# Kernel tuning notes

Measured on AMD Instinct MI355X. Metric: run time of the kernel, lower is better.

The kernel has to match this reference:

```python
import jax, jax.numpy as jnp
import numpy as np

NUM_CODEBOOKS = 8
CODEBOOK_SIZE = 2048
CODEBOOK_DIM = 16
HIDDEN_SIZE = 2048
CODEC_VOCAB_START = 0
PAD_IDX = 0


def setup_inputs() -> dict:
    key = jax.random.key(0)
    k_ids, k_emb, k_w1, k_b1, k_w2, k_b2 = jax.random.split(key, 6)
    B, S = 4, 4096
    codec_input_ids = jax.random.randint(
        k_ids, (B, S), 0, NUM_CODEBOOKS * CODEBOOK_SIZE, dtype=jnp.int64
    )
    # frozen embedding table; padding_idx row is zero
    embed_table = jax.random.normal(
        k_emb, (NUM_CODEBOOKS * CODEBOOK_SIZE, CODEBOOK_DIM), dtype=jnp.float32
    )
    embed_table = embed_table.at[PAD_IDX].set(0.0)
    # per-codebook projector params (stacked over codebook axis k)
    s1 = 1.0 / np.sqrt(CODEBOOK_DIM)
    s2 = 1.0 / np.sqrt(HIDDEN_SIZE)
    W1 = jax.random.uniform(k_w1, (NUM_CODEBOOKS, CODEBOOK_DIM, HIDDEN_SIZE), jnp.float32, -s1, s1)
    b1 = jax.random.uniform(k_b1, (NUM_CODEBOOKS, HIDDEN_SIZE), jnp.float32, -s1, s1)
    W2 = jax.random.uniform(k_w2, (NUM_CODEBOOKS, HIDDEN_SIZE, HIDDEN_SIZE), jnp.float32, -s2, s2)
    b2 = jax.random.uniform(k_b2, (NUM_CODEBOOKS, HIDDEN_SIZE), jnp.float32, -s2, s2)
    return {
        "codec_input_ids": codec_input_ids,
        "embed_table": embed_table,
        "W1": W1,
        "b1": b1,
        "W2": W2,
        "b2": b2,
    }


def reference(codec_input_ids, embed_table, W1, b1, W2, b2):
    ids = codec_input_ids - CODEC_VOCAB_START          # [B, S]
    embeds = embed_table[ids]                          # [B, S, D]
    cb = ids // CODEBOOK_SIZE                          # which codebook each token belongs to
    out = jnp.zeros(ids.shape + (HIDDEN_SIZE,), dtype=embeds.dtype)
    # fixed small loop over structurally distinct per-codebook projectors;
    # disjoint masks cover all tokens, so masked accumulation == torch scatter
    for k in range(NUM_CODEBOOKS):
        h = jnp.einsum("bsd,dh->bsh", embeds, W1[k]) + b1[k]
        h = jax.nn.gelu(h, approximate=False)          # torch nn.GELU default = exact
        h = jnp.einsum("bsh,hg->bsg", h, W2[k]) + b2[k]
        out = out + jnp.where((cb == k)[..., None], h, 0.0)
    return out
```

## Files before the change

### kernel.cpp

```cpp
#include <hip/hip_runtime.h>
#include <hip/hip_bf16.h>
#include <stdint.h>

#define NUM_CB   8
#define CB_BITS  11
#define DIM      16
#define HS       2048
#define NTOK     16384

#define BM 256
#define BN 256
#define BK 64
#define NKT (HS / BK)
#define MAXT 72
#define GEMM_GRID (8 * MAXT)

#define OFF_CUR    0u
#define OFF_NT     64u
#define OFF_GS     128u
#define OFF_TCB    256u
#define OFF_TROW   1024u
#define OFF_TVAL   2048u
#define OFF_PERM   4096u
#define OFF_H      69632u
#define OFF_W2T    67178496u
#define WS_NEED    134287360u

typedef __attribute__((ext_vector_type(8))) short s16x8;
typedef __attribute__((ext_vector_type(4))) float f32x4;

__device__ __forceinline__ void load_lds16(const void* g, const void* l) {
    __builtin_amdgcn_global_load_lds(
        (const __attribute__((address_space(1))) uint32_t*)g,
        (__attribute__((address_space(3))) uint32_t*)(void*)(uintptr_t)l, 16, 0, 0);
}

extern "C" __global__ void k_countplan(const int* __restrict__ ids,
                                       uint32_t* __restrict__ cur, uint32_t* __restrict__ numT,
                                       uint32_t* __restrict__ tcb, uint32_t* __restrict__ trow,
                                       uint32_t* __restrict__ tval, uint32_t* __restrict__ gstart) {
    __shared__ uint32_t hist[NUM_CB];
    __shared__ uint32_t s_tcb[MAXT], s_trow[MAXT], s_tval[MAXT];
    __shared__ uint32_t s_gs[NUM_CB], s_nt;
    const int tid = threadIdx.x;
    if (tid < NUM_CB) { hist[tid] = 0; cur[tid] = 0; }
    __syncthreads();
    uint32_t c0=0,c1=0,c2=0,c3=0,c4=0,c5=0,c6=0,c7=0;
    const int4* v4 = (const int4*)ids;
    for (int i = tid; i < NTOK / 4; i += 1024) {
        int4 v = v4[i];
        uint32_t a = (uint32_t)v.x >> CB_BITS, b = (uint32_t)v.y >> CB_BITS;
        uint32_t cc = (uint32_t)v.z >> CB_BITS, d = (uint32_t)v.w >> CB_BITS;
        c0 += (a==0)+(b==0)+(cc==0)+(d==0);  c1 += (a==1)+(b==1)+(cc==1)+(d==1);
        c2 += (a==2)+(b==2)+(cc==2)+(d==2);  c3 += (a==3)+(b==3)+(cc==3)+(d==3);
        c4 += (a==4)+(b==4)+(cc==4)+(d==4);  c5 += (a==5)+(b==5)+(cc==5)+(d==5);
        c6 += (a==6)+(b==6)+(cc==6)+(d==6);  c7 += (a==7)+(b==7)+(cc==7)+(d==7);
    }
    #pragma unroll
    for (int off = 32; off > 0; off >>= 1) {
        c0 += __shfl_down(c0, off); c1 += __shfl_down(c1, off);
        c2 += __shfl_down(c2, off); c3 += __shfl_down(c3, off);
        c4 += __shfl_down(c4, off); c5 += __shfl_down(c5, off);
        c6 += __shfl_down(c6, off); c7 += __shfl_down(c7, off);
    }
    if ((tid & 63) == 0) {
        if (c0) atomicAdd(&hist[0], c0); if (c1) atomicAdd(&hist[1], c1);
        if (c2) atomicAdd(&hist[2], c2); if (c3) atomicAdd(&hist[3], c3);
        if (c4) atomicAdd(&hist[4], c4); if (c5) atomicAdd(&hist[5], c5);
        if (c6) atomicAdd(&hist[6], c6); if (c7) atomicAdd(&hist[7], c7);
    }
    __syncthreads();
    if (tid == 0) {
        uint32_t ps = 0, nt = 0;
        for (int k = 0; k < NUM_CB; ++k) {
            s_gs[k] = ps;
            uint32_t c = hist[k];
            uint32_t tiles = (c + BM - 1) / BM;
            for (uint32_t m = 0; m < tiles; ++m) {
                s_tcb[nt] = (uint32_t)k;
                s_trow[nt] = ps + m * BM;
                uint32_t rem = c - m * BM;
                s_tval[nt] = rem < BM ? rem : BM;
                ++nt;
            }
            ps += c;
        }
        s_nt = nt;
    }
    __syncthreads();
    const uint32_t nt = s_nt;
    if (tid < MAXT) {
        tcb[tid]  = (tid < (int)nt) ? s_tcb[tid] : 0u;
        trow[tid] = (tid < (int)nt) ? s_trow[tid] : 0u;
        tval[tid] = (tid < (int)nt) ? s_tval[tid] : 0u;
    }
    if (tid < NUM_CB) gstart[tid] = s_gs[tid];
    if (tid == 0) *numT = nt;
}

extern "C" __global__ void k_assign(const int* __restrict__ ids, const uint32_t* __restrict__ gstart,
                                    uint32_t* __restrict__ cur, uint32_t* __restrict__ perm) {
    __shared__ uint32_t lh[NUM_CB], lbase[NUM_CB];
    const int tid = threadIdx.x;
    const int t = blockIdx.x * 256 + tid;
    if (tid < NUM_CB) lh[tid] = 0;
    __syncthreads();
    const int cb = (uint32_t)ids[t] >> CB_BITS;
    atomicAdd(&lh[cb], 1u);
    __syncthreads();
    if (tid < NUM_CB) {
        lbase[tid] = lh[tid] ? atomicAdd(&cur[tid], lh[tid]) : 0u;
        lh[tid] = 0;
    }
    __syncthreads();
    const uint32_t r = atomicAdd(&lh[cb], 1u);
    perm[gstart[cb] + lbase[cb] + r] = (uint32_t)t;
}

extern "C" __global__ void k_hbuild(const int* __restrict__ ids, const float* __restrict__ emb,
                                    const float* __restrict__ W1, const float* __restrict__ b1,
                                    const uint32_t* __restrict__ numT, const uint32_t* __restrict__ tcb,
                                    const uint32_t* __restrict__ trow, const uint32_t* __restrict__ tval,
                                    const uint32_t* __restrict__ perm, __hip_bfloat16* __restrict__ H) {
    if (blockIdx.x >= *numT) return;
    const int cb = (int)tcb[blockIdx.x];
    const int row0 = (int)trow[blockIdx.x];
    const int valid = (int)tval[blockIdx.x];
    const int col0 = blockIdx.y * 256;
    const int tid = threadIdx.x;

    __shared__ float es[BM][DIM];
    __shared__ float w1s[DIM][256];
    __shared__ int   rid[BM];

    rid[tid] = (tid < valid) ? ids[perm[row0 + tid]] : 0;
    __syncthreads();
    #pragma unroll
    for (int i = 0; i < 4; ++i) {
        int idx = i * 256 + tid;
        int r = idx >> 2, q = (idx & 3) * 4;
        *(float4*)&es[r][q] = *(const float4*)&emb[(size_t)rid[r] * DIM + q];
    }
    const float* W1k = W1 + (size_t)cb * DIM * HS + col0;
    #pragma unroll
    for (int i = 0; i < 4; ++i) {
        int idx = i * 256 + tid;
        int d = idx >> 6, c4 = (idx & 63) * 4;
        *(float4*)&w1s[d][c4] = *(const float4*)&W1k[(size_t)d * HS + c4];
    }
    __syncthreads();

    float w[DIM];
    #pragma unroll
    for (int d = 0; d < DIM; ++d) w[d] = w1s[d][tid];
    const float bb = b1[(size_t)cb * HS + col0 + tid];
    __hip_bfloat16* Hc = H + (size_t)row0 * HS + col0 + tid;

    for (int r = 0; r < BM; ++r) {
        if (r >= valid) break;
        const float4 e0 = *(const float4*)&es[r][0];
        const float4 e1 = *(const float4*)&es[r][4];
        const float4 e2 = *(const float4*)&es[r][8];
        const float4 e3 = *(const float4*)&es[r][12];
        float acc = bb;
        acc += e0.x*w[0] + e0.y*w[1] + e0.z*w[2] + e0.w*w[3];
        acc += e1.x*w[4] + e1.y*w[5] + e1.z*w[6] + e1.w*w[7];
        acc += e2.x*w[8] + e2.y*w[9] + e2.z*w[10] + e2.w*w[11];
        acc += e3.x*w[12] + e3.y*w[13] + e3.z*w[14] + e3.w*w[15];
        float g = 0.5f * acc * (1.f + erff(acc * 0.70710678118f));
        Hc[(size_t)r * HS] = __float2bfloat16(g);
    }
}

extern "C" __global__ void k_w2t(const float* __restrict__ W2, __hip_bfloat16* __restrict__ W2T) {
    __shared__ float s[64][65];
    const int k0 = blockIdx.x * 64, n0 = blockIdx.y * 64, cb = blockIdx.z;
    const int tid = threadIdx.x;
    const float* src = W2 + ((size_t)cb << 22);
    #pragma unroll
    for (int i = 0; i < 4; ++i) {
        int idx = i * 256 + tid;
        int kl = idx >> 4, n4 = (idx & 15) * 4;
        float4 v = *(const float4*)&src[(size_t)(k0 + kl) * HS + n0 + n4];
        s[kl][n4] = v.x; s[kl][n4+1] = v.y; s[kl][n4+2] = v.z; s[kl][n4+3] = v.w;
    }
    __syncthreads();
    __hip_bfloat16* dst = W2T + ((size_t)cb << 22);
    #pragma unroll
    for (int i = 0; i < 4; ++i) {
        int idx = i * 256 + tid;
        int n = idx >> 4, k4 = (idx & 15) * 4;
        __align__(8) __hip_bfloat16 o[4];
        o[0] = __float2bfloat16(s[k4+0][n]); o[1] = __float2bfloat16(s[k4+1][n]);
        o[2] = __float2bfloat16(s[k4+2][n]); o[3] = __float2bfloat16(s[k4+3][n]);
        *(ushort4*)&dst[(size_t)(n0 + n) * HS + k0 + k4] = *(const ushort4*)o;
    }
}

#define MM(m_, a_, n_, b_) acc[m_][n_] = __builtin_amdgcn_mfma_f32_16x16x32_bf16(a_, b_, acc[m_][n_], 0, 0, 0)

#define STAGE_A(q_, c47_, koff_) do {                                          \
    const unsigned short* _g = gA_t + (koff_) + (c47_) * 32;                   \
    load_lds16(_g,      sA + (q_)*32768 + (c47_)*16384 + wbase);               \
    load_lds16(_g + 16, sA + (q_)*32768 + (c47_)*16384 + wbase + 8192);        \
} while (0)
#define STAGE_B(q_, c47_, koff_) do {                                          \
    const unsigned short* _g = gB_t + (koff_) + (c47_) * 32;                   \
    load_lds16(_g,      sB + (q_)*32768 + (c47_)*16384 + wbase);               \
    load_lds16(_g + 16, sB + (q_)*32768 + (c47_)*16384 + wbase + 8192);        \
} while (0)

#define VM4 asm volatile("s_waitcnt vmcnt(4)" ::: "memory")
#define VM0 asm volatile("s_waitcnt vmcnt(0)" ::: "memory")
#define BAR __builtin_amdgcn_s_barrier()
#define LGK0 asm volatile("s_waitcnt lgkmcnt(0)" ::: "memory")
#define SCHB __builtin_amdgcn_sched_barrier(0)
#define NOSTG ((void)0)

#define PHASE_B(p_, ks_, STG) do {                                             \
    const char* Bb_ = sB + (p_)*32768 + (ks_)*16384 + laneB;                   \
    bb0 = *(const s16x8*)(Bb_);       bb1 = *(const s16x8*)(Bb_ + 256);        \
    bb2 = *(const s16x8*)(Bb_ + 512); bb3 = *(const s16x8*)(Bb_ + 768);        \
    const char* Ab_ = sA + (p_)*32768 + (ks_)*16384 + laneA;                   \
    s16x8 a0 = *(const s16x8*)(Ab_);       s16x8 a1 = *(const s16x8*)(Ab_ + 256); \
    s16x8 a2 = *(const s16x8*)(Ab_ + 512); s16x8 a3 = *(const s16x8*)(Ab_ + 768); \
    STG;                                                                       \
    __builtin_amdgcn_s_barrier();                                              \
    LGK0; SCHB;                                                                \
    __builtin_amdgcn_s_setprio(1);                                             \
    MM(0, a0, 0, bb0); MM(0, a0, 1, bb1); MM(0, a0, 2, bb2); MM(0, a0, 3, bb3);\
    MM(1, a1, 0, bb0); MM(1, a1, 1, bb1); MM(1, a1, 2, bb2); MM(1, a1, 3, bb3);\
    MM(2, a2, 0, bb0); MM(2, a2, 1, bb1); MM(2, a2, 2, bb2); MM(2, a2, 3, bb3);\
    MM(3, a3, 0, bb0); MM(3, a3, 1, bb1); MM(3, a3, 2, bb2); MM(3, a3, 3, bb3);\
    __builtin_amdgcn_s_setprio(0);                                             \
} while (0)

#define PHASE_R(p_, ks_, STG) do {                                             \
    const char* Ab_ = sA + (p_)*32768 + (ks_)*16384 + laneA + 1024;            \
    s16x8 a0 = *(const s16x8*)(Ab_);       s16x8 a1 = *(const s16x8*)(Ab_ + 256); \
    s16x8 a2 = *(const s16x8*)(Ab_ + 512); s16x8 a3 = *(const s16x8*)(Ab_ + 768); \
    STG;                                                                       \
    __builtin_amdgcn_s_barrier();                                              \
    LGK0; SCHB;                                                                \
    __builtin_amdgcn_s_setprio(1);                                             \
    MM(4, a0, 0, bb0); MM(4, a0, 1, bb1); MM(4, a0, 2, bb2); MM(4, a0, 3, bb3);\
    MM(5, a1, 0, bb0); MM(5, a1, 1, bb1); MM(5, a1, 2, bb2); MM(5, a1, 3, bb3);\
    MM(6, a2, 0, bb0); MM(6, a2, 1, bb1); MM(6, a2, 2, bb2); MM(6, a2, 3, bb3);\
    MM(7, a3, 0, bb0); MM(7, a3, 1, bb1); MM(7, a3, 2, bb2); MM(7, a3, 3, bb3);\
    __builtin_amdgcn_s_setprio(0);                                             \
} while (0)

extern "C" __global__ void __launch_bounds__(512, 2) k_gemm(
    const __hip_bfloat16* __restrict__ Hb, const __hip_bfloat16* __restrict__ W2Tb,
    const float* __restrict__ b2, const uint32_t* __restrict__ numT,
    const uint32_t* __restrict__ tcb, const uint32_t* __restrict__ trow,
    const uint32_t* __restrict__ tval, const uint32_t* __restrict__ perm,
    float* __restrict__ out)
{
    const int wg = (int)(blockIdx.x & 7) * (GEMM_GRID / 8) + (int)(blockIdx.x >> 3);
    const int mslot = wg >> 3;
    const int nb = wg & 7;
    if (mslot >= (int)*numT) return;
    const int cb = (int)tcb[mslot];
    const int row0 = (int)trow[mslot];
    const int valid = (int)tval[mslot];
    const int n0 = nb * BN;

    const int tid = threadIdx.x;
    const int lane = tid & 63, wave = tid >> 6;
    const int wm = wave >> 2, wn = wave & 3;

    __shared__ __align__(16) char sA[65536];
    __shared__ __align__(16) char sB[65536];

    const unsigned short* H  = (const unsigned short*)Hb;
    const unsigned short* W2 = (const unsigned short*)W2Tb;

    const int trl = tid & 255;
    const int rA = trl < valid ? trl : (valid - 1);
    const unsigned short* gA_t = H  + (size_t)(row0 + rA) * HS + (tid >> 8) * 8;
    const unsigned short* gB_t = W2 + ((size_t)cb * HS + n0 + trl) * HS + (tid >> 8) * 8;
    const uint32_t wbase = (uint32_t)__builtin_amdgcn_readfirstlane((uint32_t)(wave << 10));

    const uint32_t laneA = ((uint32_t)(lane >> 4) << 12) + (((uint32_t)(lane & 15) + wm * 128) << 4);
    const uint32_t laneB = ((uint32_t)(lane >> 4) << 12) + (((uint32_t)(lane & 15) + wn * 64) << 4);

    f32x4 acc[8][4];
    #pragma unroll
    for (int i = 0; i < 8; ++i)
        #pragma unroll
        for (int j = 0; j < 4; ++j) acc[i][j] = (f32x4){0.f, 0.f, 0.f, 0.f};

    s16x8 bb0, bb1, bb2, bb3;

    STAGE_A(0, 0, 0); STAGE_B(0, 0, 0); STAGE_A(0, 1, 0); STAGE_B(0, 1, 0);
    VM4;
    BAR;

    for (int kt = 0; kt < NKT - 1; ++kt) {
        const int p = kt & 1, q = p ^ 1;
        const int koff = (kt + 1) * BK;
        PHASE_B(p, 0, STAGE_A(q, 0, koff));      BAR;
        PHASE_R(p, 0, STAGE_B(q, 0, koff)); VM4; BAR;
        PHASE_B(p, 1, STAGE_A(q, 1, koff));      BAR;
        PHASE_R(p, 1, STAGE_B(q, 1, koff)); VM4; BAR;
    }
    PHASE_B(1, 0, NOSTG);      BAR;
    PHASE_R(1, 0, NOSTG); VM0; BAR;
    PHASE_B(1, 1, NOSTG);      BAR;
    PHASE_R(1, 1, NOSTG);

    const float* b2k = b2 + (size_t)cb * HS;
    const int colb = n0 + wn * 64 + (lane & 15);
    float bias[4];
    #pragma unroll
    for (int nf = 0; nf < 4; ++nf) bias[nf] = b2k[colb + nf * 16];

    #pragma unroll
    for (int mf = 0; mf < 8; ++mf) {
        #pragma unroll
        for (int jj = 0; jj < 4; ++jj) {
            const int m = wm * 128 + mf * 16 + (lane >> 4) * 4 + jj;
            if (m < valid) {
                float* op = out + (size_t)perm[row0 + m] * HS;
                #pragma unroll
                for (int nf = 0; nf < 4; ++nf)
                    op[colb + nf * 16] = acc[mf][nf][jj] + bias[nf];
            }
        }
    }
}

extern "C" void kernel_launch(void* const* d_in, const int* in_sizes, int n_in,
                              void* d_out, int out_size, void* d_ws, size_t ws_size,
                              hipStream_t stream) {
    const int*   ids = (const int*)d_in[0];
    const float* emb = (const float*)d_in[1];
    const float* W1  = (const float*)d_in[2];
    const float* b1  = (const float*)d_in[3];
    const float* W2  = (const float*)d_in[4];
    const float* b2  = (const float*)d_in[5];
    float* out = (float*)d_out;

    if (ws_size < (size_t)WS_NEED) return;

    char* ws = (char*)d_ws;
    uint32_t* cur    = (uint32_t*)(ws + OFF_CUR);
    uint32_t* numT   = (uint32_t*)(ws + OFF_NT);
    uint32_t* gstart = (uint32_t*)(ws + OFF_GS);
    uint32_t* tcb    = (uint32_t*)(ws + OFF_TCB);
    uint32_t* trow   = (uint32_t*)(ws + OFF_TROW);
    uint32_t* tval   = (uint32_t*)(ws + OFF_TVAL);
    uint32_t* perm   = (uint32_t*)(ws + OFF_PERM);
    __hip_bfloat16* Hbf  = (__hip_bfloat16*)(ws + OFF_H);
    __hip_bfloat16* W2Tb = (__hip_bfloat16*)(ws + OFF_W2T);

    k_countplan<<<1, 1024, 0, stream>>>(ids, cur, numT, tcb, trow, tval, gstart);
    k_assign   <<<NTOK / 256, 256, 0, stream>>>(ids, gstart, cur, perm);
    k_w2t      <<<dim3(32, 32, 8), 256, 0, stream>>>(W2, W2Tb);
    k_hbuild   <<<dim3(MAXT, 8), 256, 0, stream>>>(ids, emb, W1, b1, numT, tcb, trow, tval, perm, Hbf);
    k_gemm     <<<GEMM_GRID, 512, 0, stream>>>(Hbf, W2Tb, b2, numT, tcb, trow, tval, perm, out);
}
```

Before: 635.2 us.

## Replace fine-grained phased GEMM pipeline with simple per-tile double buffering

Drops the four-phase interleaved schedule, which had a barrier per phase, partial vmcnt waits, sched_barrier and setprio. It now issues all next-tile global-to-LDS loads up front, computes both k-halves of the current tile, then waits for all loads and barriers once per K tile. This removes most barriers and lets the compiler schedule the MFMAs freely. In exchange, the staggered overlap of loads with MFMAs and the priority hints are lost, and register pressure may rise because A fragments are held longer.

Measured after the change: 652.3 us. 2.7% more time.

```diff
diff --git a/kernel.cpp b/kernel.cpp
--- a/kernel.cpp
+++ b/kernel.cpp
@@ -210,44 +210,27 @@
     load_lds16(_g + 16, sB + (q_)*32768 + (c47_)*16384 + wbase + 8192);        \
 } while (0)
 
-#define VM4 asm volatile("s_waitcnt vmcnt(4)" ::: "memory")
 #define VM0 asm volatile("s_waitcnt vmcnt(0)" ::: "memory")
 #define BAR __builtin_amdgcn_s_barrier()
-#define LGK0 asm volatile("s_waitcnt lgkmcnt(0)" ::: "memory")
-#define SCHB __builtin_amdgcn_sched_barrier(0)
-#define NOSTG ((void)0)
-
-#define PHASE_B(p_, ks_, STG) do {                                             \
+
+#define KS_HALF(p_, ks_) do {                                                  \
     const char* Bb_ = sB + (p_)*32768 + (ks_)*16384 + laneB;                   \
-    bb0 = *(const s16x8*)(Bb_);       bb1 = *(const s16x8*)(Bb_ + 256);        \
-    bb2 = *(const s16x8*)(Bb_ + 512); bb3 = *(const s16x8*)(Bb_ + 768);        \
-    const char* Ab_ = sA + (p_)*32768 + (ks_)*16384 + laneA;                   \
-    s16x8 a0 = *(const s16x8*)(Ab_);       s16x8 a1 = *(const s16x8*)(Ab_ + 256); \
-    s16x8 a2 = *(const s16x8*)(Ab_ + 512); s16x8 a3 = *(const s16x8*)(Ab_ + 768); \
-    STG;                                                                       \
-    __builtin_amdgcn_s_barrier();                                              \
-    LGK0; SCHB;                                                                \
-    __builtin_amdgcn_s_setprio(1);                                             \
-    MM(0, a0, 0, bb0); MM(0, a0, 1, bb1); MM(0, a0, 2, bb2); MM(0, a0, 3, bb3);\
-    MM(1, a1, 0, bb0); MM(1, a1, 1, bb1); MM(1, a1, 2, bb2); MM(1, a1, 3, bb3);\
-    MM(2, a2, 0, bb0); MM(2, a2, 1, bb1); MM(2, a2, 2, bb2); MM(2, a2, 3, bb3);\
-    MM(3, a3, 0, bb0); MM(3, a3, 1, bb1); MM(3, a3, 2, bb2); MM(3, a3, 3, bb3);\
-    __builtin_amdgcn_s_setprio(0);                                             \
-} while (0)
-
-#define PHASE_R(p_, ks_, STG) do {                                             \
-    const char* Ab_ = sA + (p_)*32768 + (ks_)*16384 + laneA + 1024;            \
-    s16x8 a0 = *(const s16x8*)(Ab_);       s16x8 a1 = *(const s16x8*)(Ab_ + 256); \
-    s16x8 a2 = *(const s16x8*)(Ab_ + 512); s16x8 a3 = *(const s16x8*)(Ab_ + 768); \
-    STG;                                                                       \
-    __builtin_amdgcn_s_barrier();                                              \
-    LGK0; SCHB;                                                                \
-    __builtin_amdgcn_s_setprio(1);                                             \
-    MM(4, a0, 0, bb0); MM(4, a0, 1, bb1); MM(4, a0, 2, bb2); MM(4, a0, 3, bb3);\
-    MM(5, a1, 0, bb0); MM(5, a1, 1, bb1); MM(5, a1, 2, bb2); MM(5, a1, 3, bb3);\
-    MM(6, a2, 0, bb0); MM(6, a2, 1, bb1); MM(6, a2, 2, bb2); MM(6, a2, 3, bb3);\
-    MM(7, a3, 0, bb0); MM(7, a3, 1, bb1); MM(7, a3, 2, bb2); MM(7, a3, 3, bb3);\
-    __builtin_amdgcn_s_setprio(0);                                             \
+    s16x8 b0 = *(const s16x8*)(Bb_);       s16x8 b1 = *(const s16x8*)(Bb_ + 256); \
+    s16x8 b2 = *(const s16x8*)(Bb_ + 512); s16x8 b3 = *(const s16x8*)(Bb_ + 768); \
+    const char* A0_ = sA + (p_)*32768 + (ks_)*16384 + laneA;                   \
+    s16x8 a0 = *(const s16x8*)(A0_);       s16x8 a1 = *(const s16x8*)(A0_ + 256); \
+    s16x8 a2 = *(const s16x8*)(A0_ + 512); s16x8 a3 = *(const s16x8*)(A0_ + 768); \
+    MM(0, a0, 0, b0); MM(0, a0, 1, b1); MM(0, a0, 2, b2); MM(0, a0, 3, b3);    \
+    MM(1, a1, 0, b0); MM(1, a1, 1, b1); MM(1, a1, 2, b2); MM(1, a1, 3, b3);    \
+    MM(2, a2, 0, b0); MM(2, a2, 1, b1); MM(2, a2, 2, b2); MM(2, a2, 3, b3);    \
+    MM(3, a3, 0, b0); MM(3, a3, 1, b1); MM(3, a3, 2, b2); MM(3, a3, 3, b3);    \
+    const char* A1_ = A0_ + 1024;                                              \
+    s16x8 c0 = *(const s16x8*)(A1_);       s16x8 c1 = *(const s16x8*)(A1_ + 256); \
+    s16x8 c2 = *(const s16x8*)(A1_ + 512); s16x8 c3 = *(const s16x8*)(A1_ + 768); \
+    MM(4, c0, 0, b0); MM(4, c0, 1, b1); MM(4, c0, 2, b2); MM(4, c0, 3, b3);    \
+    MM(5, c1, 0, b0); MM(5, c1, 1, b1); MM(5, c1, 2, b2); MM(5, c1, 3, b3);    \
+    MM(6, c2, 0, b0); MM(6, c2, 1, b1); MM(6, c2, 2, b2); MM(6, c2, 3, b3);    \
+    MM(7, c3, 0, b0); MM(7, c3, 1, b1); MM(7, c3, 2, b2); MM(7, c3, 3, b3);    \
 } while (0)
 
 extern "C" __global__ void __launch_bounds__(512, 2) k_gemm(
@@ -291,24 +274,22 @@
         #pragma unroll
         for (int j = 0; j < 4; ++j) acc[i][j] = (f32x4){0.f, 0.f, 0.f, 0.f};
 
-    s16x8 bb0, bb1, bb2, bb3;
-
-    STAGE_A(0, 0, 0); STAGE_B(0, 0, 0); STAGE_A(0, 1, 0); STAGE_B(0, 1, 0);
-    VM4;
+    STAGE_A(0, 0, 0); STAGE_A(0, 1, 0); STAGE_B(0, 0, 0); STAGE_B(0, 1, 0);
+    VM0;
     BAR;
 
-    for (int kt = 0; kt < NKT - 1; ++kt) {
+    for (int kt = 0; kt < NKT; ++kt) {
         const int p = kt & 1, q = p ^ 1;
-        const int koff = (kt + 1) * BK;
-        PHASE_B(p, 0, STAGE_A(q, 0, koff));      BAR;
-        PHASE_R(p, 0, STAGE_B(q, 0, koff)); VM4; BAR;
-        PHASE_B(p, 1, STAGE_A(q, 1, koff));      BAR;
-        PHASE_R(p, 1, STAGE_B(q, 1, koff)); VM4; BAR;
-    }
-    PHASE_B(1, 0, NOSTG);      BAR;
-    PHASE_R(1, 0, NOSTG); VM0; BAR;
-    PHASE_B(1, 1, NOSTG);      BAR;
-    PHASE_R(1, 1, NOSTG);
+        if (kt + 1 < NKT) {
+            const int koff = (kt + 1) * BK;
+            STAGE_A(q, 0, koff); STAGE_A(q, 1, koff);
+            STAGE_B(q, 0, koff); STAGE_B(q, 1, koff);
+        }
+        KS_HALF(p, 0);
+        KS_HALF(p, 1);
+        VM0;
+        BAR;
+    }
 
     const float* b2k = b2 + (size_t)cb * HS;
     const int colb = n0 + wn * 64 + (lane & 15);
```
